# Kernel tuning notes

Hardware: AMD Instinct MI355X
Metric: run time of the kernel (lower is better)

## Reference

```python
import jax, jax.numpy as jnp
import numpy as np

PENALTY_PARAM = 0.1
NROWS, NCOLS = 256, 256
BATCH = 512


def setup_inputs() -> dict:
    key = jax.random.key(0)
    Y = jax.random.normal(key, (BATCH, NROWS * NCOLS), dtype=jnp.float32)
    return {"Y": Y}


def reference(Y):
    # Y: [B, nrows*ncols] flattened images
    img = Y.reshape(Y.shape[0], NROWS, NCOLS)  # [B, H, W]
    # vertical neighbor diffs: |y[r,c] - y[r+1,c]| for r < H-1
    vdiff = jnp.abs(img[:, :-1, :] - img[:, 1:, :])
    # horizontal neighbor diffs: |y[r,c] - y[r,c+1]| for c < W-1
    hdiff = jnp.abs(img[:, :, :-1] - img[:, :, 1:])
    abs_grad_sum = vdiff.sum(axis=(1, 2)) + hdiff.sum(axis=(1, 2))  # [B]
    areas = Y.sum(axis=1)  # [B]
    return (areas - PENALTY_PARAM * abs_grad_sum)[:, None]  # [B, 1]
```

## Files before the change

### kernel.cpp

```cpp
#include <hip/hip_runtime.h>

#define NROWS   256
#define NCOLS   256
#define PENALTY 0.1f

__global__ __launch_bounds__(256, 8) void gaau_kernel(const float* __restrict__ Y,
                                                      float* __restrict__ out) {
    const int tid  = threadIdx.x;
    const int lane = tid & 63;
    const int wave = tid >> 6;
    const int b    = blockIdx.x >> 4;
    const int band = blockIdx.x & 15;
    const int r0   = band * 16 + wave * 4;

    const float4* p4 = (const float4*)(Y + (size_t)b * (NROWS * NCOLS))
                       + r0 * (NCOLS / 4) + lane;

    float4 v0 = p4[0 * 64];
    float4 v1 = p4[1 * 64];
    float4 v2 = p4[2 * 64];
    float4 v3 = p4[3 * 64];
    float4 v4 = v3;
    if (r0 + 4 < NROWS) v4 = p4[4 * 64];

    float nx0 = __shfl_down(v0.x, 1, 64);
    float nx1 = __shfl_down(v1.x, 1, 64);
    float nx2 = __shfl_down(v2.x, 1, 64);
    float nx3 = __shfl_down(v3.x, 1, 64);

    float area = ((v0.x + v0.y) + (v0.z + v0.w)) + ((v1.x + v1.y) + (v1.z + v1.w)) +
                 ((v2.x + v2.y) + (v2.z + v2.w)) + ((v3.x + v3.y) + (v3.z + v3.w));

    float gh = (fabsf(v0.x - v0.y) + fabsf(v0.y - v0.z)) + fabsf(v0.z - v0.w) +
               (fabsf(v1.x - v1.y) + fabsf(v1.y - v1.z)) + fabsf(v1.z - v1.w) +
               (fabsf(v2.x - v2.y) + fabsf(v2.y - v2.z)) + fabsf(v2.z - v2.w) +
               (fabsf(v3.x - v3.y) + fabsf(v3.y - v3.z)) + fabsf(v3.z - v3.w);
    if (lane < 63)
        gh += (fabsf(v0.w - nx0) + fabsf(v1.w - nx1)) +
              (fabsf(v2.w - nx2) + fabsf(v3.w - nx3));

    float gv = (fabsf(v0.x - v1.x) + fabsf(v0.y - v1.y)) +
               (fabsf(v0.z - v1.z) + fabsf(v0.w - v1.w)) +
               (fabsf(v1.x - v2.x) + fabsf(v1.y - v2.y)) +
               (fabsf(v1.z - v2.z) + fabsf(v1.w - v2.w)) +
               (fabsf(v2.x - v3.x) + fabsf(v2.y - v3.y)) +
               (fabsf(v2.z - v3.z) + fabsf(v2.w - v3.w)) +
               (fabsf(v3.x - v4.x) + fabsf(v3.y - v4.y)) +
               (fabsf(v3.z - v4.z) + fabsf(v3.w - v4.w));

    float val = area - PENALTY * (gh + gv);

    #pragma unroll
    for (int off = 32; off > 0; off >>= 1)
        val += __shfl_down(val, off, 64);

    __shared__ float sm[4];
    if (lane == 0) sm[wave] = val;
    __syncthreads();

    if (tid == 0) {
        float s = (sm[0] + sm[1]) + (sm[2] + sm[3]);
        atomicAdd(out + b, s);
    }
}

extern "C" void kernel_launch(void* const* d_in, const int* in_sizes, int n_in,
                              void* d_out, int out_size, void* d_ws, size_t ws_size,
                              hipStream_t stream) {
    const float* Y  = (const float*)d_in[0];
    float* out      = (float*)d_out;
    const int batch = in_sizes[0] / (NROWS * NCOLS);
    gaau_kernel<<<batch * 16, 256, 0, stream>>>(Y, out);
}
```

Before: 184.8 us.

## Process 16 rows per wave with software-prefetched chunks and fewer blocks

Each wave now covers 16 rows instead of 4, walking through four 4-row chunks and loading the next chunk before computing on the current one, so the row shared with the next chunk is reused rather than reloaded. Blocks per image drop from 16 to 4, which cuts the redundant halo-row loads and the number of atomic adds to the output by a factor of four. Launch bounds are relaxed to 4 blocks per CU to allow more registers for the prefetch. The cost is fewer blocks overall and less occupancy to hide memory latency.

```diff
diff --git a/kernel.cpp b/kernel.cpp
--- a/kernel.cpp
+++ b/kernel.cpp
@@ -4,49 +4,70 @@
 #define NCOLS   256
 #define PENALTY 0.1f
 
-__global__ __launch_bounds__(256, 8) void gaau_kernel(const float* __restrict__ Y,
+
+__device__ __forceinline__ float hsum4(float4 v) {
+    return (v.x + v.y) + (v.z + v.w);
+}
+__device__ __forceinline__ float hdiff_in(float4 v) {
+    return (fabsf(v.x - v.y) + fabsf(v.y - v.z)) + fabsf(v.z - v.w);
+}
+__device__ __forceinline__ float vdiff4(float4 a, float4 b) {
+    return (fabsf(a.x - b.x) + fabsf(a.y - b.y)) +
+           (fabsf(a.z - b.z) + fabsf(a.w - b.w));
+}
+
+__global__ __launch_bounds__(256, 4) void gaau_kernel(const float* __restrict__ Y,
                                                       float* __restrict__ out) {
     const int tid  = threadIdx.x;
     const int lane = tid & 63;
     const int wave = tid >> 6;
-    const int b    = blockIdx.x >> 4;
-    const int band = blockIdx.x & 15;
-    const int r0   = band * 16 + wave * 4;
+    const int b    = blockIdx.x >> 2;
+    const int band = blockIdx.x & 3;
+    const int r0   = band * 64 + wave * 16;
 
     const float4* p4 = (const float4*)(Y + (size_t)b * (NROWS * NCOLS))
                        + r0 * (NCOLS / 4) + lane;
 
-    float4 v0 = p4[0 * 64];
-    float4 v1 = p4[1 * 64];
-    float4 v2 = p4[2 * 64];
-    float4 v3 = p4[3 * 64];
-    float4 v4 = v3;
-    if (r0 + 4 < NROWS) v4 = p4[4 * 64];
+    float4 c0 = p4[0 * 64];
+    float4 c1 = p4[1 * 64];
+    float4 c2 = p4[2 * 64];
+    float4 c3 = p4[3 * 64];
 
-    float nx0 = __shfl_down(v0.x, 1, 64);
-    float nx1 = __shfl_down(v1.x, 1, 64);
-    float nx2 = __shfl_down(v2.x, 1, 64);
-    float nx3 = __shfl_down(v3.x, 1, 64);
+    const bool has_boundary = (r0 + 16) < NROWS;
 
-    float area = ((v0.x + v0.y) + (v0.z + v0.w)) + ((v1.x + v1.y) + (v1.z + v1.w)) +
-                 ((v2.x + v2.y) + (v2.z + v2.w)) + ((v3.x + v3.y) + (v3.z + v3.w));
+    float area = 0.0f, gh = 0.0f, gv = 0.0f;
 
-    float gh = (fabsf(v0.x - v0.y) + fabsf(v0.y - v0.z)) + fabsf(v0.z - v0.w) +
-               (fabsf(v1.x - v1.y) + fabsf(v1.y - v1.z)) + fabsf(v1.z - v1.w) +
-               (fabsf(v2.x - v2.y) + fabsf(v2.y - v2.z)) + fabsf(v2.z - v2.w) +
-               (fabsf(v3.x - v3.y) + fabsf(v3.y - v3.z)) + fabsf(v3.z - v3.w);
-    if (lane < 63)
-        gh += (fabsf(v0.w - nx0) + fabsf(v1.w - nx1)) +
-              (fabsf(v2.w - nx2) + fabsf(v3.w - nx3));
+    #pragma unroll
+    for (int c = 0; c < 4; ++c) {
+        float4 n0, n1, n2, n3;
+        if (c < 3) {
+            const float4* q = p4 + (c * 4 + 4) * 64;
+            n0 = q[0 * 64];
+            n1 = q[1 * 64];
+            n2 = q[2 * 64];
+            n3 = q[3 * 64];
+        } else {
+            n0 = c3;
+            if (has_boundary) n0 = p4[16 * 64];
+            n1 = n2 = n3 = n0;
+        }
 
-    float gv = (fabsf(v0.x - v1.x) + fabsf(v0.y - v1.y)) +
-               (fabsf(v0.z - v1.z) + fabsf(v0.w - v1.w)) +
-               (fabsf(v1.x - v2.x) + fabsf(v1.y - v2.y)) +
-               (fabsf(v1.z - v2.z) + fabsf(v1.w - v2.w)) +
-               (fabsf(v2.x - v3.x) + fabsf(v2.y - v3.y)) +
-               (fabsf(v2.z - v3.z) + fabsf(v2.w - v3.w)) +
-               (fabsf(v3.x - v4.x) + fabsf(v3.y - v4.y)) +
-               (fabsf(v3.z - v4.z) + fabsf(v3.w - v4.w));
+        area += (hsum4(c0) + hsum4(c1)) + (hsum4(c2) + hsum4(c3));
+
+        gh += (hdiff_in(c0) + hdiff_in(c1)) + (hdiff_in(c2) + hdiff_in(c3));
+        float nx0 = __shfl_down(c0.x, 1, 64);
+        float nx1 = __shfl_down(c1.x, 1, 64);
+        float nx2 = __shfl_down(c2.x, 1, 64);
+        float nx3 = __shfl_down(c3.x, 1, 64);
+        if (lane < 63)
+            gh += (fabsf(c0.w - nx0) + fabsf(c1.w - nx1)) +
+                  (fabsf(c2.w - nx2) + fabsf(c3.w - nx3));
+
+        gv += (vdiff4(c0, c1) + vdiff4(c1, c2)) +
+              (vdiff4(c2, c3) + vdiff4(c3, n0));
+
+        c0 = n0; c1 = n1; c2 = n2; c3 = n3;
+    }
 
     float val = area - PENALTY * (gh + gv);
 
@@ -70,5 +91,5 @@
     const float* Y  = (const float*)d_in[0];
     float* out      = (float*)d_out;
     const int batch = in_sizes[0] / (NROWS * NCOLS);
-    gaau_kernel<<<batch * 16, 256, 0, stream>>>(Y, out);
+    gaau_kernel<<<batch * 4, 256, 0, stream>>>(Y, out);
 }
```

Measured after the change: 186.5 us. No clear change (+0.9%).
